# Performance work log

Measured on AMD Instinct MI355X. Metric: run time of the kernel, lower is better.

The kernel has to match this reference:

```python
import jax, jax.numpy as jnp
import numpy as np

B, C, H, W = 16, 32, 32, 2048


def setup_inputs() -> dict:
    key = jax.random.key(0)
    ks = jax.random.split(key, 7)
    s = 1.0 / np.sqrt(C * H)  # torch conv2d default init scale (fan_in = C*H*1)
    x = jax.random.normal(ks[0], (B, C, H, W), dtype=jnp.float32)
    wq = jax.random.uniform(ks[1], (C, C, H), jnp.float32, -s, s)
    bq = jax.random.uniform(ks[2], (C,), jnp.float32, -s, s)
    wk = jax.random.uniform(ks[3], (C, C, H), jnp.float32, -s, s)
    bk = jax.random.uniform(ks[4], (C,), jnp.float32, -s, s)
    wv = jax.random.uniform(ks[5], (C, C, H), jnp.float32, -s, s)
    bv = jax.random.uniform(ks[6], (C,), jnp.float32, -s, s)
    return {"x": x, "wq": wq, "bq": bq, "wk": wk, "bk": bk, "wv": wv, "bv": bv}


def _proj(x, w, b):
    # Conv2d kernel (H,1) with no padding == contract over (in_channels, H).
    # x: [B,C,H,W], w: [Cout,Cin,H] -> [B,Cout,W]
    return jnp.einsum('bihw,oih->bow', x, w) + b[None, :, None]


def reference(x, wq, bq, wk, bk, wv, bv):
    q = _proj(x, wq, bq)            # [B,C,W]
    k = _proj(x, wk, bk)            # [B,C,W]
    v = _proj(x, wv, bv)            # [B,C,W]
    # query.permute(0,2,1) @ key -> [B,W,W]; NOTE: unscaled, as in source.
    scores = jnp.einsum('bcw,bcv->bwv', q, k)
    attn = jax.nn.softmax(scores, axis=-1)
    # value @ attention^T -> [B,C,W]
    out = jnp.einsum('bcv,bwv->bcw', v, attn)
    # bilinear upsample (1,W)->(H,W), align_corners=False: width is identity,
    # height replicates the single row -> pure broadcast. Then residual add.
    return out[:, :, None, :] + x
```

## Files before the change

### kernel.cpp

```cpp
#include <hip/hip_runtime.h>
#include <hip/hip_bf16.h>

typedef __bf16 bf16x8 __attribute__((ext_vector_type(8)));
typedef float  f32x4  __attribute__((ext_vector_type(4)));
typedef float  f32x16 __attribute__((ext_vector_type(16)));

#define NB 16
#define NC 32
#define NH 32
#define NW 2048
#define NK (NC*NH)
#define LOG2E 1.4426950408889634f
#define TPAD 1040

static __device__ __forceinline__ unsigned int pk2(float a, float b) {
    union { __bf16 h[2]; unsigned int u; } z;
    z.h[0] = (__bf16)a; z.h[1] = (__bf16)b;
    return z.u;
}

__global__ __launch_bounds__(256) void wprep_kernel(
    const float* __restrict__ wq, const float* __restrict__ wk,
    const float* __restrict__ wv, __bf16* __restrict__ wb)
{
    const int i = blockIdx.x * 256 + threadIdx.x;
    const float* srcs[3] = { wq, wk, wv };
    float4 v = *(const float4*)(srcs[i >> 13] + (size_t)(i & 8191) * 4);
    const float sc = (i >> 13) == 0 ? LOG2E : 1.0f;
    union { __bf16 h[4]; unsigned long long u; } z;
    z.h[0] = (__bf16)(v.x * sc); z.h[1] = (__bf16)(v.y * sc);
    z.h[2] = (__bf16)(v.z * sc); z.h[3] = (__bf16)(v.w * sc);
    *(unsigned long long*)(wb + (size_t)i * 4) = z.u;
}

__global__ __launch_bounds__(256) void proj_kernel(
    const float* __restrict__ x, const __bf16* __restrict__ wb,
    const float* __restrict__ bq, const float* __restrict__ bk,
    const float* __restrict__ bv,
    __bf16* __restrict__ qT, __bf16* __restrict__ kT, __bf16* __restrict__ V)
{
    const int b    = blockIdx.x >> 6;
    const int wt   = blockIdx.x & 63;
    const int wave = threadIdx.x >> 6;
    const int lane = threadIdx.x & 63;
    const int g    = lane >> 4;
    const int lr   = lane & 15;
    const int w0   = wt * 32;

    __shared__ __align__(16) char smem_raw[32 * TPAD * 2];
    __bf16 (*tile)[TPAD] = reinterpret_cast<__bf16(*)[TPAD]>(smem_raw);
    f32x4 (*part)[6][64] = reinterpret_cast<f32x4(*)[6][64]>(smem_raw);

    const float* xb = x + (size_t)b * NK * NW;

    {
        const int swq = threadIdx.x & 7;
        const int skr = threadIdx.x >> 3;
        const float* xs = xb + w0 + swq * 4;
        __bf16* wp0 = &tile[swq * 4][skr];
        #pragma unroll 8
        for (int pass = 0; pass < 32; ++pass) {
            const int k = pass * 32 + skr;
            const float4 v = *(const float4*)(xs + (size_t)k * NW);
            __bf16* wp = wp0 + pass * 32;
            wp[0*TPAD] = (__bf16)v.x;
            wp[1*TPAD] = (__bf16)v.y;
            wp[2*TPAD] = (__bf16)v.z;
            wp[3*TPAD] = (__bf16)v.w;
        }
    }
    __syncthreads();

    const int k0 = wave * 256;
    f32x4 acc[2][6];
    #pragma unroll
    for (int mt = 0; mt < 2; ++mt)
        #pragma unroll
        for (int nt = 0; nt < 6; ++nt)
            acc[mt][nt] = f32x4{0.f, 0.f, 0.f, 0.f};

    #pragma unroll
    for (int s = 0; s < 8; ++s) {
        const int kk = k0 + s * 32;
        const bf16x8 af0 = *(const bf16x8*)&tile[lr][kk + g*8];
        const bf16x8 af1 = *(const bf16x8*)&tile[16 + lr][kk + g*8];
        bf16x8 bfv[6];
        #pragma unroll
        for (int nt = 0; nt < 6; ++nt)
            bfv[nt] = *(const bf16x8*)(wb + (size_t)(nt >> 1) * 32768
                                          + (size_t)((nt & 1) * 16 + lr) * NK
                                          + kk + g*8);
        #pragma unroll
        for (int nt = 0; nt < 6; ++nt) {
            acc[0][nt] = __builtin_amdgcn_mfma_f32_16x16x32_bf16(
                af0, bfv[nt], acc[0][nt], 0, 0, 0);
            acc[1][nt] = __builtin_amdgcn_mfma_f32_16x16x32_bf16(
                af1, bfv[nt], acc[1][nt], 0, 0, 0);
        }
    }

    const float* biases[3] = { bq, bk, bv };
    #pragma unroll
    for (int mt = 0; mt < 2; ++mt) {
        __syncthreads();
        #pragma unroll
        for (int nt = 0; nt < 6; ++nt)
            part[wave][nt][lane] = acc[mt][nt];
        __syncthreads();
        #pragma unroll
        for (int q = 0; q < 2; ++q) {
            const int nt = wave + q * 4;
            if (nt < 6) {
                f32x4 s = part[0][nt][lane];
                #pragma unroll
                for (int sl = 1; sl < 4; ++sl) s += part[sl][nt][lane];
                const int pid = nt >> 1;
                const int o   = (nt & 1) * 16 + lr;
                float bb = biases[pid][o];
                if (pid == 0) bb *= LOG2E;
                if (pid < 2) {
                    __bf16* dst = (pid ? kT : qT) + (size_t)b * NW * NC;
                    #pragma unroll
                    for (int r = 0; r < 4; ++r) {
                        const int w = w0 + mt*16 + g*4 + r;
                        dst[(size_t)w * NC + o] = (__bf16)(s[r] + bb);
                    }
                } else {
                    union { __bf16 h[4]; unsigned long long u; } z;
                    #pragma unroll
                    for (int r = 0; r < 4; ++r) z.h[r] = (__bf16)(s[r] + bb);
                    __bf16* dst = V + ((size_t)b * NC + o) * NW + (w0 + mt*16 + g*4);
                    *(unsigned long long*)dst = z.u;
                }
            }
        }
    }
}

__global__ __launch_bounds__(256) void attn_kernel(
    const float* __restrict__ x,
    const __bf16* __restrict__ qT, const __bf16* __restrict__ kT,
    const __bf16* __restrict__ V,
    float* __restrict__ out)
{
    const int b    = blockIdx.x >> 6;
    const int wt   = blockIdx.x & 63;
    const int w0   = wt * 32;
    const int wave = threadIdx.x >> 6;
    const int lane = threadIdx.x & 63;
    const int wl = lane & 31, hi = lane >> 5;
    const int swl = (wl & 0x13) | ((wl & 4) << 1) | ((wl & 8) >> 1);

    const __bf16* qTb = qT + (size_t)b * NW * NC;
    const __bf16* kTb = kT + (size_t)b * NW * NC;
    const __bf16* Vb  = V  + (size_t)b * NC * NW;

    const __bf16* qrow = qTb + (size_t)(w0 + wl) * NC;
    const bf16x8 qf0 = *(const bf16x8*)(qrow + hi*8);
    const bf16x8 qf1 = *(const bf16x8*)(qrow + 16 + hi*8);

    f32x16 acc, z16;
    #pragma unroll
    for (int r = 0; r < 16; ++r) { acc[r] = 0.f; z16[r] = 0.f; }
    float lsum = 0.f;

    const int vbeg = wave * 512;
    const __bf16* kbase = kTb + (size_t)swl * NC;
    const __bf16* vbase = Vb + (size_t)wl * NW;

#define KLD0(V0) (*(const bf16x8*)(kbase + (size_t)(V0) * NC + hi*8))
#define KLD1(V0) (*(const bf16x8*)(kbase + (size_t)(V0) * NC + 16 + hi*8))
#define VLD0(V0) (*(const bf16x8*)(vbase + (V0) + hi*8))
#define VLD1(V0) (*(const bf16x8*)(vbase + (V0) + 16 + hi*8))

    bf16x8 k0r = KLD0(vbeg), k1r = KLD1(vbeg);
    f32x16 s_cur = __builtin_amdgcn_mfma_f32_32x32x16_bf16(k0r, qf0, z16, 0, 0, 0);
    s_cur = __builtin_amdgcn_mfma_f32_32x32x16_bf16(k1r, qf1, s_cur, 0, 0, 0);
    k0r = KLD0(vbeg + 32); k1r = KLD1(vbeg + 32);
    bf16x8 v0r = VLD0(vbeg), v1r = VLD1(vbeg);

    #pragma unroll
    for (int it = 0; it < 16; ++it) {
        f32x16 s_next;
        if (it < 15) {
            s_next = __builtin_amdgcn_mfma_f32_32x32x16_bf16(k0r, qf0, z16, 0, 0, 0);
            s_next = __builtin_amdgcn_mfma_f32_32x32x16_bf16(k1r, qf1, s_next, 0, 0, 0);
        }
        if (it < 14) {
            const int vn = vbeg + (it + 2) * 32;
            k0r = KLD0(vn); k1r = KLD1(vn);
        }

        float p[16];
        #pragma unroll
        for (int r = 0; r < 16; ++r) p[r] = __builtin_amdgcn_exp2f(s_cur[r]);
        float ts[8];
        #pragma unroll
        for (int r = 0; r < 8; ++r) ts[r] = p[r] + p[r+8];
        #pragma unroll
        for (int r = 0; r < 4; ++r) ts[r] += ts[r+4];
        lsum += (ts[0] + ts[1]) + (ts[2] + ts[3]);

        union { unsigned int u[4]; bf16x8 v; } pfa, pfb;
        #pragma unroll
        for (int i = 0; i < 4; ++i) pfa.u[i] = pk2(p[2*i],     p[2*i + 1]);
        #pragma unroll
        for (int i = 0; i < 4; ++i) pfb.u[i] = pk2(p[8 + 2*i], p[8 + 2*i + 1]);

        acc = __builtin_amdgcn_mfma_f32_32x32x16_bf16(v0r, pfa.v, acc, 0, 0, 0);
        acc = __builtin_amdgcn_mfma_f32_32x32x16_bf16(v1r, pfb.v, acc, 0, 0, 0);

        if (it < 15) {
            const int vn = vbeg + (it + 1) * 32;
            v0r = VLD0(vn); v1r = VLD1(vn);
            s_cur = s_next;
        }
    }
#undef KLD0
#undef KLD1
#undef VLD0
#undef VLD1
    lsum += __shfl_xor(lsum, 32);

    __shared__ float sl[4][32];
    __shared__ float sO[4][32][33];
    __shared__ float Of[32][33];

    if (hi == 0) sl[wave][wl] = lsum;
    #pragma unroll
    for (int r = 0; r < 16; ++r) {
        const int c = (r & 3) + 8*(r >> 2) + 4*hi;
        sO[wave][c][wl] = acc[r];
    }
    __syncthreads();

    {
        const int w  = threadIdx.x & 31;
        const int cg = threadIdx.x >> 5;
        const float L = (sl[0][w] + sl[1][w]) + (sl[2][w] + sl[3][w]);
        const float rL = 1.0f / L;
        #pragma unroll
        for (int cc = 0; cc < 4; ++cc) {
            const int c = cg * 4 + cc;
            const float o = ((sO[0][c][w] + sO[1][c][w]) +
                             (sO[2][c][w] + sO[3][c][w]));
            Of[c][w] = o * rL;
        }
    }
    __syncthreads();

    const float* xb = x   + (size_t)b * NC * NH * NW + w0;
    float*       ob = out + (size_t)b * NC * NH * NW + w0;
    const int chunk = threadIdx.x & 7;
    #pragma unroll
    for (int it = 0; it < 32; ++it) {
        const int row = it*32 + (threadIdx.x >> 3);
        const int c = row >> 5, h = row & 31;
        const size_t off = ((size_t)c * NH + h) * NW + chunk*4;
        const f32x4 xv = *(const f32x4*)(xb + off);
        f32x4 ov;
        ov[0] = Of[c][chunk*4 + 0] + xv[0];
        ov[1] = Of[c][chunk*4 + 1] + xv[1];
        ov[2] = Of[c][chunk*4 + 2] + xv[2];
        ov[3] = Of[c][chunk*4 + 3] + xv[3];
        __builtin_nontemporal_store(ov, (f32x4*)(ob + off));
    }
}

extern "C" void kernel_launch(void* const* d_in, const int* in_sizes, int n_in,
                              void* d_out, int out_size, void* d_ws, size_t ws_size,
                              hipStream_t stream)
{
    const float* x  = (const float*)d_in[0];
    const float* wq = (const float*)d_in[1];
    const float* bq = (const float*)d_in[2];
    const float* wk = (const float*)d_in[3];
    const float* bk = (const float*)d_in[4];
    const float* wv = (const float*)d_in[5];
    const float* bv = (const float*)d_in[6];
    float* out = (float*)d_out;

    char* ws = (char*)d_ws;
    __bf16* qT = (__bf16*)(ws);
    __bf16* kT = (__bf16*)(ws + (2u << 20));
    __bf16* V  = (__bf16*)(ws + (4u << 20));
    __bf16* wb = (__bf16*)(ws + (6u << 20));

    hipLaunchKernelGGL(wprep_kernel, dim3(96), dim3(256), 0, stream, wq, wk, wv, wb);
    hipLaunchKernelGGL(proj_kernel, dim3(NB * 64), dim3(256), 0, stream,
                       x, wb, bq, bk, bv, qT, kT, V);
    hipLaunchKernelGGL(attn_kernel, dim3(NB * 64), dim3(256), 0, stream,
                       x, qT, kT, V, out);
}
```

Measured before the change: 109.1 us.

## Drop LDS staging in projection, convert weights inline, add separate V transpose

The projection kernel no longer stages x through a large padded LDS tile. It reads x straight from global memory with strided scalar loads and converts to bf16 in registers. The fp32 weights are also converted and scaled inline, which removes the separate weight-prep kernel. V is now written in the same transposed layout as q and k and fixed up by a new small transpose kernel, replacing the narrow V writes. This trades LDS capacity and a launch for uncoalesced strided x reads, repeated weight conversion in every block, and an extra kernel plus round trip for V.

```diff
diff --git a/kernel.cpp b/kernel.cpp
--- a/kernel.cpp
+++ b/kernel.cpp
@@ -11,7 +11,6 @@
 #define NW 2048
 #define NK (NC*NH)
 #define LOG2E 1.4426950408889634f
-#define TPAD 1040
 
 static __device__ __forceinline__ unsigned int pk2(float a, float b) {
     union { __bf16 h[2]; unsigned int u; } z;
@@ -19,25 +18,12 @@
     return z.u;
 }
 
-__global__ __launch_bounds__(256) void wprep_kernel(
-    const float* __restrict__ wq, const float* __restrict__ wk,
-    const float* __restrict__ wv, __bf16* __restrict__ wb)
-{
-    const int i = blockIdx.x * 256 + threadIdx.x;
-    const float* srcs[3] = { wq, wk, wv };
-    float4 v = *(const float4*)(srcs[i >> 13] + (size_t)(i & 8191) * 4);
-    const float sc = (i >> 13) == 0 ? LOG2E : 1.0f;
-    union { __bf16 h[4]; unsigned long long u; } z;
-    z.h[0] = (__bf16)(v.x * sc); z.h[1] = (__bf16)(v.y * sc);
-    z.h[2] = (__bf16)(v.z * sc); z.h[3] = (__bf16)(v.w * sc);
-    *(unsigned long long*)(wb + (size_t)i * 4) = z.u;
-}
-
 __global__ __launch_bounds__(256) void proj_kernel(
-    const float* __restrict__ x, const __bf16* __restrict__ wb,
-    const float* __restrict__ bq, const float* __restrict__ bk,
-    const float* __restrict__ bv,
-    __bf16* __restrict__ qT, __bf16* __restrict__ kT, __bf16* __restrict__ V)
+    const float* __restrict__ x,
+    const float* __restrict__ wq, const float* __restrict__ bq,
+    const float* __restrict__ wk, const float* __restrict__ bk,
+    const float* __restrict__ wv, const float* __restrict__ bv,
+    __bf16* __restrict__ qT, __bf16* __restrict__ kT, __bf16* __restrict__ vT)
 {
     const int b    = blockIdx.x >> 6;
     const int wt   = blockIdx.x & 63;
@@ -47,31 +33,10 @@
     const int lr   = lane & 15;
     const int w0   = wt * 32;
 
-    __shared__ __align__(16) char smem_raw[32 * TPAD * 2];
-    __bf16 (*tile)[TPAD] = reinterpret_cast<__bf16(*)[TPAD]>(smem_raw);
-    f32x4 (*part)[6][64] = reinterpret_cast<f32x4(*)[6][64]>(smem_raw);
-
     const float* xb = x + (size_t)b * NK * NW;
-
-    {
-        const int swq = threadIdx.x & 7;
-        const int skr = threadIdx.x >> 3;
-        const float* xs = xb + w0 + swq * 4;
-        __bf16* wp0 = &tile[swq * 4][skr];
-        #pragma unroll 8
-        for (int pass = 0; pass < 32; ++pass) {
-            const int k = pass * 32 + skr;
-            const float4 v = *(const float4*)(xs + (size_t)k * NW);
-            __bf16* wp = wp0 + pass * 32;
-            wp[0*TPAD] = (__bf16)v.x;
-            wp[1*TPAD] = (__bf16)v.y;
-            wp[2*TPAD] = (__bf16)v.z;
-            wp[3*TPAD] = (__bf16)v.w;
-        }
-    }
-    __syncthreads();
-
+    const float* wptr[6] = { wq, wq + 16*NK, wk, wk + 16*NK, wv, wv + 16*NK };
     const int k0 = wave * 256;
+
     f32x4 acc[2][6];
     #pragma unroll
     for (int mt = 0; mt < 2; ++mt)
@@ -79,61 +44,89 @@
         for (int nt = 0; nt < 6; ++nt)
             acc[mt][nt] = f32x4{0.f, 0.f, 0.f, 0.f};
 
-    #pragma unroll
-    for (int s = 0; s < 8; ++s) {
-        const int kk = k0 + s * 32;
-        const bf16x8 af0 = *(const bf16x8*)&tile[lr][kk + g*8];
-        const bf16x8 af1 = *(const bf16x8*)&tile[16 + lr][kk + g*8];
+    for (int ki = 0; ki < 8; ++ki) {
+        const int kk = k0 + ki * 32;
+        bf16x8 af[2];
+        #pragma unroll
+        for (int mt = 0; mt < 2; ++mt) {
+            const float* p = xb + (size_t)(kk + g*8) * NW + (w0 + mt*16 + lr);
+            bf16x8 t;
+            #pragma unroll
+            for (int j = 0; j < 8; ++j) t[j] = (__bf16)p[(size_t)j * NW];
+            af[mt] = t;
+        }
         bf16x8 bfv[6];
         #pragma unroll
+        for (int nt = 0; nt < 6; ++nt) {
+            const float sc = (nt < 2) ? LOG2E : 1.0f;
+            const float* p = wptr[nt] + (size_t)lr * NK + kk + g*8;
+            float4 lo = *(const float4*)p;
+            float4 hi = *(const float4*)(p + 4);
+            bf16x8 t;
+            t[0]=(__bf16)(lo.x*sc); t[1]=(__bf16)(lo.y*sc);
+            t[2]=(__bf16)(lo.z*sc); t[3]=(__bf16)(lo.w*sc);
+            t[4]=(__bf16)(hi.x*sc); t[5]=(__bf16)(hi.y*sc);
+            t[6]=(__bf16)(hi.z*sc); t[7]=(__bf16)(hi.w*sc);
+            bfv[nt] = t;
+        }
+        #pragma unroll
+        for (int mt = 0; mt < 2; ++mt)
+            #pragma unroll
+            for (int nt = 0; nt < 6; ++nt)
+                acc[mt][nt] = __builtin_amdgcn_mfma_f32_16x16x32_bf16(
+                    af[mt], bfv[nt], acc[mt][nt], 0, 0, 0);
+    }
+
+    __shared__ f32x4 part[4][12][64];
+    #pragma unroll
+    for (int mt = 0; mt < 2; ++mt)
+        #pragma unroll
         for (int nt = 0; nt < 6; ++nt)
-            bfv[nt] = *(const bf16x8*)(wb + (size_t)(nt >> 1) * 32768
-                                          + (size_t)((nt & 1) * 16 + lr) * NK
-                                          + kk + g*8);
-        #pragma unroll
-        for (int nt = 0; nt < 6; ++nt) {
-            acc[0][nt] = __builtin_amdgcn_mfma_f32_16x16x32_bf16(
-                af0, bfv[nt], acc[0][nt], 0, 0, 0);
-            acc[1][nt] = __builtin_amdgcn_mfma_f32_16x16x32_bf16(
-                af1, bfv[nt], acc[1][nt], 0, 0, 0);
-        }
-    }
-
+            part[wave][mt*6 + nt][lane] = acc[mt][nt];
+    __syncthreads();
+
+    const int mt     = wave & 1;
+    const int ntbase = (wave >> 1) * 3;
     const float* biases[3] = { bq, bk, bv };
     #pragma unroll
-    for (int mt = 0; mt < 2; ++mt) {
-        __syncthreads();
-        #pragma unroll
-        for (int nt = 0; nt < 6; ++nt)
-            part[wave][nt][lane] = acc[mt][nt];
-        __syncthreads();
-        #pragma unroll
-        for (int q = 0; q < 2; ++q) {
-            const int nt = wave + q * 4;
-            if (nt < 6) {
-                f32x4 s = part[0][nt][lane];
-                #pragma unroll
-                for (int sl = 1; sl < 4; ++sl) s += part[sl][nt][lane];
-                const int pid = nt >> 1;
-                const int o   = (nt & 1) * 16 + lr;
-                float bb = biases[pid][o];
-                if (pid == 0) bb *= LOG2E;
-                if (pid < 2) {
-                    __bf16* dst = (pid ? kT : qT) + (size_t)b * NW * NC;
-                    #pragma unroll
-                    for (int r = 0; r < 4; ++r) {
-                        const int w = w0 + mt*16 + g*4 + r;
-                        dst[(size_t)w * NC + o] = (__bf16)(s[r] + bb);
-                    }
-                } else {
-                    union { __bf16 h[4]; unsigned long long u; } z;
-                    #pragma unroll
-                    for (int r = 0; r < 4; ++r) z.h[r] = (__bf16)(s[r] + bb);
-                    __bf16* dst = V + ((size_t)b * NC + o) * NW + (w0 + mt*16 + g*4);
-                    *(unsigned long long*)dst = z.u;
-                }
-            }
-        }
+    for (int nti = 0; nti < 3; ++nti) {
+        const int nt = ntbase + nti;
+        const int fi = mt*6 + nt;
+        f32x4 s = part[0][fi][lane];
+        #pragma unroll
+        for (int sl = 1; sl < 4; ++sl) s += part[sl][fi][lane];
+        const int pid = nt >> 1;
+        const int o   = (nt & 1) * 16 + lr;
+        float bb = biases[pid][o];
+        if (pid == 0) bb *= LOG2E;
+        __bf16* dst = (pid == 0 ? qT : pid == 1 ? kT : vT) + (size_t)b * NW * NC;
+        #pragma unroll
+        for (int r = 0; r < 4; ++r) {
+            const int w = w0 + mt*16 + g*4 + r;
+            dst[(size_t)w * NC + o] = (__bf16)(s[r] + bb);
+        }
+    }
+}
+
+__global__ __launch_bounds__(256) void vtrans_kernel(
+    const __bf16* __restrict__ vT, __bf16* __restrict__ V)
+{
+    __shared__ __bf16 t[NC][136];
+    const int b  = blockIdx.x >> 4;
+    const int wc = blockIdx.x & 15;
+    const int w0 = wc * 128;
+    #pragma unroll
+    for (int e = 0; e < 16; ++e) {
+        int flat = e*256 + threadIdx.x;
+        int wl = flat >> 5, c = flat & 31;
+        t[c][wl] = vT[((size_t)b*NW + w0 + wl) * NC + c];
+    }
+    __syncthreads();
+    #pragma unroll
+    for (int e = 0; e < 16; ++e) {
+        int flat = e*256 + threadIdx.x;
+        int c = flat >> 7, wl = flat & 127;
+        V[((size_t)b*NC + c) * NW + w0 + wl] = t[c][wl];
     }
 }
 
@@ -283,12 +276,12 @@
     char* ws = (char*)d_ws;
     __bf16* qT = (__bf16*)(ws);
     __bf16* kT = (__bf16*)(ws + (2u << 20));
-    __bf16* V  = (__bf16*)(ws + (4u << 20));
-    __bf16* wb = (__bf16*)(ws + (6u << 20));
-
-    hipLaunchKernelGGL(wprep_kernel, dim3(96), dim3(256), 0, stream, wq, wk, wv, wb);
+    __bf16* vT = (__bf16*)(ws + (4u << 20));
+    __bf16* V  = (__bf16*)(ws + (6u << 20));
+
     hipLaunchKernelGGL(proj_kernel, dim3(NB * 64), dim3(256), 0, stream,
-                       x, wb, bq, bk, bv, qT, kT, V);
+                       x, wq, bq, wk, bk, wv, bv, qT, kT, vT);
+    hipLaunchKernelGGL(vtrans_kernel, dim3(NB * 16), dim3(256), 0, stream, vT, V);
     hipLaunchKernelGGL(attn_kernel, dim3(NB * 64), dim3(256), 0, stream,
                        x, qT, kT, V, out);
 }
```

Measured after the change: 115.1 us. +5.5%, slower.

## Restructure projection kernel into double-buffered K-loop with one output tile per wave

Applied to the files above, without the earlier changes.

The projection kernel no longer stages the whole 32x1024 x tile into shared memory, which needed about 66KB of LDS. It now streams K in 32-wide chunks through a small double-buffered LDS tile, prefetching the next x chunk and the next weight fragment while the MFMAs for the current chunk run. Blocks grow to 6 waves, each owning one 16-column output tile over the full K, so the cross-wave LDS reduction goes away. The cost is 32 block-wide barriers per block and fewer independent MFMAs per wave to hide latency, but the much smaller LDS footprint should allow higher occupancy.

```diff
diff --git a/kernel.cpp b/kernel.cpp
--- a/kernel.cpp
+++ b/kernel.cpp
@@ -11,7 +11,7 @@
 #define NW 2048
 #define NK (NC*NH)
 #define LOG2E 1.4426950408889634f
-#define TPAD 1040
+#define KP 40
 
 static __device__ __forceinline__ unsigned int pk2(float a, float b) {
     union { __bf16 h[2]; unsigned int u; } z;
@@ -33,7 +33,7 @@
     *(unsigned long long*)(wb + (size_t)i * 4) = z.u;
 }
 
-__global__ __launch_bounds__(256) void proj_kernel(
+__global__ __launch_bounds__(384) void proj_kernel(
     const float* __restrict__ x, const __bf16* __restrict__ wb,
     const float* __restrict__ bq, const float* __restrict__ bk,
     const float* __restrict__ bv,
@@ -41,99 +41,82 @@
 {
     const int b    = blockIdx.x >> 6;
     const int wt   = blockIdx.x & 63;
-    const int wave = threadIdx.x >> 6;
+    const int nt   = threadIdx.x >> 6;
     const int lane = threadIdx.x & 63;
     const int g    = lane >> 4;
     const int lr   = lane & 15;
     const int w0   = wt * 32;
 
-    __shared__ __align__(16) char smem_raw[32 * TPAD * 2];
-    __bf16 (*tile)[TPAD] = reinterpret_cast<__bf16(*)[TPAD]>(smem_raw);
-    f32x4 (*part)[6][64] = reinterpret_cast<f32x4(*)[6][64]>(smem_raw);
+    __shared__ __bf16 tile[2][32][KP];
 
     const float* xb = x + (size_t)b * NK * NW;
 
-    {
-        const int swq = threadIdx.x & 7;
-        const int skr = threadIdx.x >> 3;
-        const float* xs = xb + w0 + swq * 4;
-        __bf16* wp0 = &tile[swq * 4][skr];
-        #pragma unroll 8
-        for (int pass = 0; pass < 32; ++pass) {
-            const int k = pass * 32 + skr;
-            const float4 v = *(const float4*)(xs + (size_t)k * NW);
-            __bf16* wp = wp0 + pass * 32;
-            wp[0*TPAD] = (__bf16)v.x;
-            wp[1*TPAD] = (__bf16)v.y;
-            wp[2*TPAD] = (__bf16)v.z;
-            wp[3*TPAD] = (__bf16)v.w;
-        }
-    }
+    const int skr = threadIdx.x >> 3;
+    const int swc = (threadIdx.x & 7) * 4;
+    const bool stager = (threadIdx.x < 256);
+    const float* xs = xb + w0 + swc;
+
+    const __bf16* wrow = wb + (size_t)(nt >> 1) * 32768
+                            + (size_t)((nt & 1) * 16 + lr) * NK;
+
+    f32x4 acc0 = {0.f,0.f,0.f,0.f}, acc1 = {0.f,0.f,0.f,0.f};
+
+    f32x4 xv;
+    if (stager) {
+        xv = *(const f32x4*)(xs + (size_t)skr * NW);
+        __bf16* wp = &tile[0][swc][skr];
+        wp[0*KP] = (__bf16)xv[0]; wp[1*KP] = (__bf16)xv[1];
+        wp[2*KP] = (__bf16)xv[2]; wp[3*KP] = (__bf16)xv[3];
+    }
+    bf16x8 Bcur = *(const bf16x8*)(wrow + g*8);
     __syncthreads();
 
-    const int k0 = wave * 256;
-    f32x4 acc[2][6];
-    #pragma unroll
-    for (int mt = 0; mt < 2; ++mt)
-        #pragma unroll
-        for (int nt = 0; nt < 6; ++nt)
-            acc[mt][nt] = f32x4{0.f, 0.f, 0.f, 0.f};
-
-    #pragma unroll
-    for (int s = 0; s < 8; ++s) {
-        const int kk = k0 + s * 32;
-        const bf16x8 af0 = *(const bf16x8*)&tile[lr][kk + g*8];
-        const bf16x8 af1 = *(const bf16x8*)&tile[16 + lr][kk + g*8];
-        bf16x8 bfv[6];
-        #pragma unroll
-        for (int nt = 0; nt < 6; ++nt)
-            bfv[nt] = *(const bf16x8*)(wb + (size_t)(nt >> 1) * 32768
-                                          + (size_t)((nt & 1) * 16 + lr) * NK
-                                          + kk + g*8);
-        #pragma unroll
-        for (int nt = 0; nt < 6; ++nt) {
-            acc[0][nt] = __builtin_amdgcn_mfma_f32_16x16x32_bf16(
-                af0, bfv[nt], acc[0][nt], 0, 0, 0);
-            acc[1][nt] = __builtin_amdgcn_mfma_f32_16x16x32_bf16(
-                af1, bfv[nt], acc[1][nt], 0, 0, 0);
-        }
-    }
-
+    for (int s = 0; s < 32; ++s) {
+        const int cur = s & 1;
+        f32x4 xn;
+        if (s < 31 && stager)
+            xn = *(const f32x4*)(xs + (size_t)((s+1)*32 + skr) * NW);
+        bf16x8 Bnext;
+        if (s < 31)
+            Bnext = *(const bf16x8*)(wrow + (s+1)*32 + g*8);
+
+        const bf16x8 af0 = *(const bf16x8*)&tile[cur][lr][g*8];
+        const bf16x8 af1 = *(const bf16x8*)&tile[cur][16 + lr][g*8];
+        acc0 = __builtin_amdgcn_mfma_f32_16x16x32_bf16(af0, Bcur, acc0, 0, 0, 0);
+        acc1 = __builtin_amdgcn_mfma_f32_16x16x32_bf16(af1, Bcur, acc1, 0, 0, 0);
+
+        if (s < 31 && stager) {
+            __bf16* wp = &tile[cur ^ 1][swc][skr];
+            wp[0*KP] = (__bf16)xn[0]; wp[1*KP] = (__bf16)xn[1];
+            wp[2*KP] = (__bf16)xn[2]; wp[3*KP] = (__bf16)xn[3];
+        }
+        Bcur = Bnext;
+        __syncthreads();
+    }
+
+    const int pid = nt >> 1;
+    const int o   = (nt & 1) * 16 + lr;
     const float* biases[3] = { bq, bk, bv };
-    #pragma unroll
-    for (int mt = 0; mt < 2; ++mt) {
-        __syncthreads();
-        #pragma unroll
-        for (int nt = 0; nt < 6; ++nt)
-            part[wave][nt][lane] = acc[mt][nt];
-        __syncthreads();
-        #pragma unroll
-        for (int q = 0; q < 2; ++q) {
-            const int nt = wave + q * 4;
-            if (nt < 6) {
-                f32x4 s = part[0][nt][lane];
-                #pragma unroll
-                for (int sl = 1; sl < 4; ++sl) s += part[sl][nt][lane];
-                const int pid = nt >> 1;
-                const int o   = (nt & 1) * 16 + lr;
-                float bb = biases[pid][o];
-                if (pid == 0) bb *= LOG2E;
-                if (pid < 2) {
-                    __bf16* dst = (pid ? kT : qT) + (size_t)b * NW * NC;
-                    #pragma unroll
-                    for (int r = 0; r < 4; ++r) {
-                        const int w = w0 + mt*16 + g*4 + r;
-                        dst[(size_t)w * NC + o] = (__bf16)(s[r] + bb);
-                    }
-                } else {
-                    union { __bf16 h[4]; unsigned long long u; } z;
-                    #pragma unroll
-                    for (int r = 0; r < 4; ++r) z.h[r] = (__bf16)(s[r] + bb);
-                    __bf16* dst = V + ((size_t)b * NC + o) * NW + (w0 + mt*16 + g*4);
-                    *(unsigned long long*)dst = z.u;
-                }
-            }
-        }
+    float bb = biases[pid][o];
+    if (pid == 0) bb *= LOG2E;
+
+    if (pid < 2) {
+        __bf16* dst = (pid ? kT : qT) + (size_t)b * NW * NC;
+        #pragma unroll
+        for (int r = 0; r < 4; ++r) {
+            dst[(size_t)(w0 +      g*4 + r) * NC + o] = (__bf16)(acc0[r] + bb);
+            dst[(size_t)(w0 + 16 + g*4 + r) * NC + o] = (__bf16)(acc1[r] + bb);
+        }
+    } else {
+        __bf16* dst = V + ((size_t)b * NC + o) * NW + w0;
+        union { __bf16 h[4]; unsigned long long u; } z0, z1;
+        #pragma unroll
+        for (int r = 0; r < 4; ++r) {
+            z0.h[r] = (__bf16)(acc0[r] + bb);
+            z1.h[r] = (__bf16)(acc1[r] + bb);
+        }
+        *(unsigned long long*)(dst +      g*4) = z0.u;
+        *(unsigned long long*)(dst + 16 + g*4) = z1.u;
     }
 }
 
@@ -287,7 +270,7 @@
     __bf16* wb = (__bf16*)(ws + (6u << 20));
 
     hipLaunchKernelGGL(wprep_kernel, dim3(96), dim3(256), 0, stream, wq, wk, wv, wb);
-    hipLaunchKernelGGL(proj_kernel, dim3(NB * 64), dim3(256), 0, stream,
+    hipLaunchKernelGGL(proj_kernel, dim3(NB * 64), dim3(384), 0, stream,
                        x, wb, bq, bk, bv, qT, kT, V);
     hipLaunchKernelGGL(attn_kernel, dim3(NB * 64), dim3(256), 0, stream,
                        x, qT, kT, V, out);
```

After: 93.92 us. 13.9% less time.

## Stream x tiles into LDS via global_load_lds double buffering in proj kernel

Applied to the files above, without the earlier changes.

Replaces the up-front cooperative load of the whole 32x1024 x tile (converted to bf16 in LDS) with per-wave, double-buffered direct global-to-LDS loads of fp32 chunks using an XOR swizzle. The weight operand loads are software-pipelined one step ahead in registers. The bf16 conversion now happens when each fragment is read from LDS. The aim is to overlap global loads with MFMA work and drop the block-wide barrier after staging. In exchange it relies on hand-written vmcnt waits, and the scalar LDS reads with conversion may add instruction overhead.

```diff
diff --git a/kernel.cpp b/kernel.cpp
--- a/kernel.cpp
+++ b/kernel.cpp
@@ -11,7 +11,6 @@
 #define NW 2048
 #define NK (NC*NH)
 #define LOG2E 1.4426950408889634f
-#define TPAD 1040
 
 static __device__ __forceinline__ unsigned int pk2(float a, float b) {
     union { __bf16 h[2]; unsigned int u; } z;
@@ -47,31 +46,20 @@
     const int lr   = lane & 15;
     const int w0   = wt * 32;
 
-    __shared__ __align__(16) char smem_raw[32 * TPAD * 2];
-    __bf16 (*tile)[TPAD] = reinterpret_cast<__bf16(*)[TPAD]>(smem_raw);
-    f32x4 (*part)[6][64] = reinterpret_cast<f32x4(*)[6][64]>(smem_raw);
+    __shared__ __align__(16) char smem[32768];
+    f32x4 (*part)[6][64] = reinterpret_cast<f32x4(*)[6][64]>(smem);
 
     const float* xb = x + (size_t)b * NK * NW;
-
-    {
-        const int swq = threadIdx.x & 7;
-        const int skr = threadIdx.x >> 3;
-        const float* xs = xb + w0 + swq * 4;
-        __bf16* wp0 = &tile[swq * 4][skr];
-        #pragma unroll 8
-        for (int pass = 0; pass < 32; ++pass) {
-            const int k = pass * 32 + skr;
-            const float4 v = *(const float4*)(xs + (size_t)k * NW);
-            __bf16* wp = wp0 + pass * 32;
-            wp[0*TPAD] = (__bf16)v.x;
-            wp[1*TPAD] = (__bf16)v.y;
-            wp[2*TPAD] = (__bf16)v.z;
-            wp[3*TPAD] = (__bf16)v.w;
-        }
-    }
-    __syncthreads();
-
     const int k0 = wave * 256;
+
+    const int drow = lane >> 3;
+    const int dch  = (lane & 7) ^ drow;
+    const float* xsrc = xb + w0 + dch * 4;
+
+    char* wbase = smem + wave * 8192;
+
+    const __bf16* wrow = wb + (size_t)0;
+
     f32x4 acc[2][6];
     #pragma unroll
     for (int mt = 0; mt < 2; ++mt)
@@ -79,25 +67,62 @@
         for (int nt = 0; nt < 6; ++nt)
             acc[mt][nt] = f32x4{0.f, 0.f, 0.f, 0.f};
 
+    bf16x8 Bcur[6], Bnxt[6];
+
+#define DMA(S)                                                                \
+    { char* dst = wbase + ((S) & 1) * 4096;                                   \
+      _Pragma("unroll")                                                       \
+      for (int jc = 0; jc < 4; ++jc) {                                        \
+          const float* gs = xsrc + (size_t)(k0 + (S)*32 + jc*8 + drow) * NW;  \
+          __builtin_amdgcn_global_load_lds(                                   \
+              (const __attribute__((address_space(1))) unsigned int*)gs,     \
+              (__attribute__((address_space(3))) unsigned int*)(dst + jc*1024),\
+              16, 0, 0);                                                      \
+      } }
+
+#define BLOAD(DST, S)                                                         \
+    _Pragma("unroll")                                                         \
+    for (int nt = 0; nt < 6; ++nt)                                            \
+        DST[nt] = *(const bf16x8*)(wb + (size_t)(nt >> 1) * 32768             \
+                                      + (size_t)((nt & 1) * 16 + lr) * NK     \
+                                      + k0 + (S)*32 + g*8);
+
+    DMA(0);
+    BLOAD(Bcur, 0);
+
     #pragma unroll
     for (int s = 0; s < 8; ++s) {
-        const int kk = k0 + s * 32;
-        const bf16x8 af0 = *(const bf16x8*)&tile[lr][kk + g*8];
-        const bf16x8 af1 = *(const bf16x8*)&tile[16 + lr][kk + g*8];
-        bf16x8 bfv[6];
-        #pragma unroll
-        for (int nt = 0; nt < 6; ++nt)
-            bfv[nt] = *(const bf16x8*)(wb + (size_t)(nt >> 1) * 32768
-                                          + (size_t)((nt & 1) * 16 + lr) * NK
-                                          + kk + g*8);
+        if (s < 7) { DMA(s + 1); BLOAD(Bnxt, s + 1); }
+        if (s < 7) asm volatile("s_waitcnt vmcnt(10)" ::: "memory");
+        else       asm volatile("s_waitcnt vmcnt(0)"  ::: "memory");
+        __builtin_amdgcn_sched_barrier(0);
+
+        const float* tb = (const float*)(wbase + (s & 1) * 4096);
+        bf16x8 af[2];
+        #pragma unroll
+        for (int mt = 0; mt < 2; ++mt) {
+            const int c = mt*4 + (lr >> 2);
+            const int o = lr & 3;
+            #pragma unroll
+            for (int j = 0; j < 8; ++j) {
+                const float v = tb[(g*8 + j)*32 + ((c ^ j) << 2) + o];
+                af[mt][j] = (__bf16)v;
+            }
+        }
         #pragma unroll
         for (int nt = 0; nt < 6; ++nt) {
             acc[0][nt] = __builtin_amdgcn_mfma_f32_16x16x32_bf16(
-                af0, bfv[nt], acc[0][nt], 0, 0, 0);
+                af[0], Bcur[nt], acc[0][nt], 0, 0, 0);
             acc[1][nt] = __builtin_amdgcn_mfma_f32_16x16x32_bf16(
-                af1, bfv[nt], acc[1][nt], 0, 0, 0);
-        }
-    }
+                af[1], Bcur[nt], acc[1][nt], 0, 0, 0);
+        }
+        if (s < 7) {
+            #pragma unroll
+            for (int nt = 0; nt < 6; ++nt) Bcur[nt] = Bnxt[nt];
+        }
+    }
+#undef DMA
+#undef BLOAD
 
     const float* biases[3] = { bq, bk, bv };
     #pragma unroll
```

After: 97.39 us. 1.12x faster.
